# Kernel optimization log

Measured on AMD Instinct MI355X. Metric: run time of the kernel, lower is better.

## Reference

```python
import jax, jax.numpy as jnp
import numpy as np

RESERVOIR_SIZE = 2048
EMBED = 768
N_FRAMES = 256
NUM_CLASSES = 1000
BATCH = 128
SPARSITY = 0.05
SPECTRAL_RADIUS = 0.8


def _init_reservoir(key):
    k1, k2 = jax.random.split(key)
    w = jax.random.normal(k1, (RESERVOIR_SIZE, RESERVOIR_SIZE), dtype=jnp.float32)
    mask = (jax.random.uniform(k2, (RESERVOIR_SIZE, RESERVOIR_SIZE)) < SPARSITY).astype(jnp.float32)
    r = w * mask
    # rescale so spectral radius == SPECTRAL_RADIUS (matches torch eigvals-based init)
    eig = np.linalg.eigvals(np.asarray(r))
    max_abs = np.abs(eig).max()
    return r * (SPECTRAL_RADIUS / jnp.float32(max_abs))


def setup_inputs() -> dict:
    key = jax.random.key(0)
    kx, kr, kin, kout = jax.random.split(key, 4)
    x = jax.random.normal(kx, (BATCH, N_FRAMES, EMBED), dtype=jnp.float32)
    reservoir = _init_reservoir(kr)
    W_in = jax.random.normal(kin, (RESERVOIR_SIZE, EMBED), dtype=jnp.float32) * 0.1
    W_out = jax.random.normal(kout, (NUM_CLASSES, RESERVOIR_SIZE), dtype=jnp.float32) * 0.02
    b_out = jnp.zeros((NUM_CLASSES,), dtype=jnp.float32)
    return {"x": x, "reservoir": reservoir, "W_in": W_in, "W_out": W_out, "b_out": b_out}


def reference(x, reservoir, W_in, W_out, b_out):
    # x: [B, T, E]. Precompute input projections for all frames in one GEMM:
    # u[t] = x[:, t] @ W_in.T  -> [T, B, R]
    u = jnp.einsum("bte,re->tbr", x, W_in)
    state0 = jnp.zeros((x.shape[0], reservoir.shape[0]), dtype=x.dtype)

    def step(state, u_t):
        new_state = jnp.tanh(state @ reservoir.T + u_t)
        return new_state, None

    state, _ = jax.lax.scan(step, state0, u)
    # linear head (dropout is identity in eval mode)
    logits = state @ W_out.T + b_out
    return logits
```

## Files before the change

### kernel.cpp

```cpp
#include <hip/hip_runtime.h>
#include <stdint.h>
#include <stddef.h>

#define BATCH 128
#define NFRAMES 256
#define EMBED 768
#define RES 2048
#define NCLS 1000
#define NWG 256

typedef __attribute__((ext_vector_type(8))) short bf16x8;
typedef __attribute__((ext_vector_type(4))) float f32x4;
typedef unsigned short u16;

__device__ inline u16 f2bf(float f) {
    union { float f; unsigned u; } v; v.f = f;
    unsigned r = v.u + 0x7FFFu + ((v.u >> 16) & 1u);
    return (u16)(r >> 16);
}
__device__ inline float bf2f(u16 h) {
    union { unsigned u; float f; } v; v.u = ((unsigned)h) << 16;
    return v.f;
}
__device__ inline float tanh_fast(float x) {
    float z = __builtin_amdgcn_exp2f(x * 2.885390081777927f);
    return 1.f - 2.f * __builtin_amdgcn_rcpf(z + 1.f);
}

__global__ __launch_bounds__(256) void cvt_kernel(const float* __restrict__ in,
                                                  u16* __restrict__ out, int n4) {
    int i = blockIdx.x * blockDim.x + threadIdx.x;
    int stride = gridDim.x * blockDim.x;
    for (; i < n4; i += stride) {
        float4 v = ((const float4*)in)[i];
        ushort4 o;
        o.x = f2bf(v.x); o.y = f2bf(v.y); o.z = f2bf(v.z); o.w = f2bf(v.w);
        ((ushort4*)out)[i] = o;
    }
}

__global__ __launch_bounds__(512, 1) void recur_kernel(const u16* __restrict__ res,
                                                       const u16* __restrict__ win,
                                                       const u16* __restrict__ xb,
                                                       u16* __restrict__ ring,
                                                       const u16* __restrict__ s0,
                                                       unsigned* __restrict__ flags) {
    __shared__ float part[8][16][66];
    const int lane = threadIdx.x & 63;
    const int w = threadIdx.x >> 6;
    const int rowgrp = (int)(blockIdx.x & 7);
    const int colblk = (int)(blockIdx.x >> 3);
    const int m0 = rowgrp * 16;
    const int n0 = colblk * 64;
    const int lr = lane & 15;
    const int lk = (lane >> 4) * 8;
    const int rb = (lane >> 4) * 4;
    const int kbase = w * 256;
    const int xkbase = w * 96;
    unsigned* myflag = flags + rowgrp * 32 + colblk;
    const unsigned* pollflag = flags + rowgrp * 32 + (lane & 31);

    bf16x8 bfr[4][8];
#pragma unroll
    for (int jf = 0; jf < 4; jf++)
#pragma unroll
        for (int kk = 0; kk < 8; kk++)
            bfr[jf][kk] = *(const bf16x8*)(res + (size_t)(n0 + jf * 16 + lr) * RES + kbase + kk * 32 + lk);

    bf16x8 wfr[4][3];
#pragma unroll
    for (int jf = 0; jf < 4; jf++)
#pragma unroll
        for (int j = 0; j < 3; j++)
            wfr[jf][j] = *(const bf16x8*)(win + (size_t)(n0 + jf * 16 + lr) * EMBED + xkbase + j * 32 + lk);

    const int er = threadIdx.x >> 5;
    const int ec = (threadIdx.x & 31) * 2;
    const size_t gidx = (size_t)(m0 + er) * RES + n0 + ec;
    const u16* xrow = xb + (size_t)(m0 + lr) * NFRAMES * EMBED + xkbase + lk;

    for (int t = 0; t < NFRAMES; t++) {
        const u16* sin = (t == 0) ? s0 : ring + (size_t)(t - 1) * BATCH * RES;
        u16* sout = ring + (size_t)t * BATCH * RES;
        const u16* abase = sin + (size_t)(m0 + lr) * RES + kbase + lk;
        const u16* xp = xrow + (size_t)t * EMBED;

        bf16x8 xa[3];
#pragma unroll
        for (int j = 0; j < 3; j++)
            asm volatile("global_load_dwordx4 %0, %1, off"
                         : "=v"(xa[j]) : "v"(xp + j * 32));
        bf16x8 a[8];
#pragma unroll
        for (int kk = 0; kk < 8; kk++)
            asm volatile("global_load_dwordx4 %0, %1, off"
                         : "=v"(a[kk]) : "v"(abase + kk * 32));

        f32x4 acc[4];
#pragma unroll
        for (int jf = 0; jf < 4; jf++) acc[jf] = (f32x4)0.f;

        asm volatile("s_waitcnt vmcnt(8)" ::: "memory");
        __builtin_amdgcn_sched_barrier(0);
#pragma unroll
        for (int j = 0; j < 3; j++)
#pragma unroll
            for (int jf = 0; jf < 4; jf++)
                acc[jf] = __builtin_amdgcn_mfma_f32_16x16x32_bf16(xa[j], wfr[jf][j], acc[jf], 0, 0, 0);

        asm volatile("s_waitcnt vmcnt(4)" ::: "memory");
        __builtin_amdgcn_sched_barrier(0);
#pragma unroll
        for (int kk = 0; kk < 4; kk++)
#pragma unroll
            for (int jf = 0; jf < 4; jf++)
                acc[jf] = __builtin_amdgcn_mfma_f32_16x16x32_bf16(a[kk], bfr[jf][kk], acc[jf], 0, 0, 0);
        asm volatile("s_waitcnt vmcnt(0)" ::: "memory");
        __builtin_amdgcn_sched_barrier(0);
#pragma unroll
        for (int kk = 4; kk < 8; kk++)
#pragma unroll
            for (int jf = 0; jf < 4; jf++)
                acc[jf] = __builtin_amdgcn_mfma_f32_16x16x32_bf16(a[kk], bfr[jf][kk], acc[jf], 0, 0, 0);

#pragma unroll
        for (int jf = 0; jf < 4; jf++)
#pragma unroll
            for (int q = 0; q < 4; q++)
                part[w][rb + q][jf * 16 + lr] = acc[jf][q];
        __syncthreads();

        float sx = 0.f, sy = 0.f;
#pragma unroll
        for (int ww = 0; ww < 8; ww++) {
            float2 v = *(const float2*)&part[ww][er][ec];
            sx += v.x; sy += v.y;
        }
        float v0 = tanh_fast(sx);
        float v1 = tanh_fast(sy);
        unsigned pk = (unsigned)f2bf(v0) | ((unsigned)f2bf(v1) << 16);
        asm volatile("global_store_dword %0, %1, off sc0 sc1"
                     :: "v"(sout + gidx), "v"(pk) : "memory");

        asm volatile("s_waitcnt vmcnt(0)" ::: "memory");
        __syncthreads();
        if (t != NFRAMES - 1) {
            unsigned stamp = (unsigned)(t + 1);
            if (w == 0) {
                if (lane == 0)
                    asm volatile("global_store_dword %0, %1, off sc0 sc1"
                                 :: "v"(myflag), "v"(stamp) : "memory");
                unsigned f;
                do {
                    asm volatile("global_load_dword %0, %1, off sc0 sc1\n\ts_waitcnt vmcnt(0)"
                                 : "=v"(f) : "v"(pollflag) : "memory");
                    if (__all((int)(f >= stamp))) break;
                    __builtin_amdgcn_s_sleep(2);
                } while (1);
            }
            __syncthreads();
        }
    }
}

__global__ __launch_bounds__(512) void head_kernel(const u16* __restrict__ sin,
                                                   const u16* __restrict__ wout,
                                                   const float* __restrict__ bias,
                                                   float* __restrict__ out) {
    __shared__ float part[8][32][33];
    int lane = threadIdx.x & 63;
    int w = threadIdx.x >> 6;
    int m0 = blockIdx.x * 32;
    int n0 = blockIdx.y * 32;
    int k0 = w * 256;
    int lr = lane & 15;
    int lk = (lane >> 4) * 8;

    f32x4 acc[2][2];
#pragma unroll
    for (int i = 0; i < 2; i++)
#pragma unroll
        for (int j = 0; j < 2; j++) acc[i][j] = (f32x4)0.f;

    for (int kk = k0; kk < k0 + 256; kk += 32) {
        bf16x8 a[2], b[2];
#pragma unroll
        for (int i = 0; i < 2; i++)
            a[i] = *(const bf16x8*)(sin + (size_t)(m0 + i * 16 + lr) * RES + kk + lk);
#pragma unroll
        for (int j = 0; j < 2; j++) {
            int row = n0 + j * 16 + lr;
            if (row > NCLS - 1) row = NCLS - 1;
            b[j] = *(const bf16x8*)(wout + (size_t)row * RES + kk + lk);
        }
#pragma unroll
        for (int i = 0; i < 2; i++)
#pragma unroll
            for (int j = 0; j < 2; j++)
                acc[i][j] = __builtin_amdgcn_mfma_f32_16x16x32_bf16(a[i], b[j], acc[i][j], 0, 0, 0);
    }

    int rowbase = (lane >> 4) * 4;
#pragma unroll
    for (int i = 0; i < 2; i++)
#pragma unroll
        for (int j = 0; j < 2; j++)
#pragma unroll
            for (int q = 0; q < 4; q++)
                part[w][i * 16 + rowbase + q][j * 16 + lr] = acc[i][j][q];

    __syncthreads();

    for (int idx = threadIdx.x; idx < 1024; idx += 512) {
        int r = idx >> 5, c = idx & 31;
        float s = 0.f;
#pragma unroll
        for (int ww = 0; ww < 8; ww++) s += part[ww][r][c];
        int cg = n0 + c;
        if (cg < NCLS)
            out[(size_t)(m0 + r) * NCLS + cg] = s + bias[cg];
    }
}

extern "C" void kernel_launch(void* const* d_in, const int* in_sizes, int n_in,
                              void* d_out, int out_size, void* d_ws, size_t ws_size,
                              hipStream_t stream) {
    const float* x_f    = (const float*)d_in[0];
    const float* res_f  = (const float*)d_in[1];
    const float* win_f  = (const float*)d_in[2];
    const float* wout_f = (const float*)d_in[3];
    const float* bias   = (const float*)d_in[4];
    float* out = (float*)d_out;

    char* ws = (char*)d_ws;
    size_t off = 0;
    auto alloc = [&](size_t bytes) -> void* {
        void* p = ws + off;
        off += (bytes + 255) & ~(size_t)255;
        return p;
    };
    u16* res_b  = (u16*)alloc((size_t)RES * RES * 2);
    u16* win_b  = (u16*)alloc((size_t)RES * EMBED * 2);
    u16* wout_b = (u16*)alloc((size_t)NCLS * RES * 2);
    u16* x_b    = (u16*)alloc((size_t)BATCH * NFRAMES * EMBED * 2);
    u16* ring   = (u16*)alloc((size_t)NFRAMES * BATCH * RES * 2);
    u16* s0     = (u16*)alloc((size_t)BATCH * RES * 2);
    unsigned* flags = (unsigned*)alloc(1024);

    cvt_kernel<<<dim3(1024), dim3(256), 0, stream>>>(res_f, res_b, RES * RES / 4);
    cvt_kernel<<<dim3(512), dim3(256), 0, stream>>>(win_f, win_b, RES * EMBED / 4);
    cvt_kernel<<<dim3(512), dim3(256), 0, stream>>>(wout_f, wout_b, NCLS * RES / 4);
    cvt_kernel<<<dim3(2048), dim3(256), 0, stream>>>(x_f, x_b, BATCH * NFRAMES * EMBED / 4);

    hipMemsetAsync(s0, 0, (size_t)BATCH * RES * 2, stream);
    hipMemsetAsync(flags, 0, 1024, stream);

    void* args[] = { (void*)&res_b, (void*)&win_b, (void*)&x_b, (void*)&ring,
                     (void*)&s0, (void*)&flags };
    hipLaunchCooperativeKernel((const void*)recur_kernel, dim3(NWG), dim3(512),
                               args, 0, stream);

    const u16* sfin = ring + (size_t)(NFRAMES - 1) * BATCH * RES;
    head_kernel<<<dim3(4, 32), dim3(512), 0, stream>>>(sfin, wout_b, bias, out);
}
```

Before: 1.220 ms.

## Replace flag barrier with data-sentinel polling on ring buffer

Drops the per-step flag store and poll barrier between workgroups. Instead the whole ring buffer is filled with 0xFF and consumers spin until the state values they load contain no all-ones words, so the data itself serves as the readiness signal. This removes a flag round-trip and a block barrier from each timestep. In exchange it adds a 128MB memset, reloads whole tiles while polling, and relies on tanh outputs never packing to 0xFFFFFFFF plus on the order in which the bf16 pairs become visible.

```diff
diff --git a/kernel.cpp b/kernel.cpp
--- a/kernel.cpp
+++ b/kernel.cpp
@@ -17,10 +17,6 @@
     union { float f; unsigned u; } v; v.f = f;
     unsigned r = v.u + 0x7FFFu + ((v.u >> 16) & 1u);
     return (u16)(r >> 16);
-}
-__device__ inline float bf2f(u16 h) {
-    union { unsigned u; float f; } v; v.u = ((unsigned)h) << 16;
-    return v.f;
 }
 __device__ inline float tanh_fast(float x) {
     float z = __builtin_amdgcn_exp2f(x * 2.885390081777927f);
@@ -43,8 +39,7 @@
                                                        const u16* __restrict__ win,
                                                        const u16* __restrict__ xb,
                                                        u16* __restrict__ ring,
-                                                       const u16* __restrict__ s0,
-                                                       unsigned* __restrict__ flags) {
+                                                       const u16* __restrict__ s0) {
     __shared__ float part[8][16][66];
     const int lane = threadIdx.x & 63;
     const int w = threadIdx.x >> 6;
@@ -57,8 +52,6 @@
     const int rb = (lane >> 4) * 4;
     const int kbase = w * 256;
     const int xkbase = w * 96;
-    unsigned* myflag = flags + rowgrp * 32 + colblk;
-    const unsigned* pollflag = flags + rowgrp * 32 + (lane & 31);
 
     bf16x8 bfr[4][8];
 #pragma unroll
@@ -85,16 +78,16 @@
         const u16* abase = sin + (size_t)(m0 + lr) * RES + kbase + lk;
         const u16* xp = xrow + (size_t)t * EMBED;
 
+        bf16x8 a[8];
+#pragma unroll
+        for (int kk = 0; kk < 8; kk++)
+            asm volatile("global_load_dwordx4 %0, %1, off sc0 sc1"
+                         : "=v"(a[kk]) : "v"(abase + kk * 32));
         bf16x8 xa[3];
 #pragma unroll
         for (int j = 0; j < 3; j++)
             asm volatile("global_load_dwordx4 %0, %1, off"
                          : "=v"(xa[j]) : "v"(xp + j * 32));
-        bf16x8 a[8];
-#pragma unroll
-        for (int kk = 0; kk < 8; kk++)
-            asm volatile("global_load_dwordx4 %0, %1, off"
-                         : "=v"(a[kk]) : "v"(abase + kk * 32));
 
         f32x4 acc[4];
 #pragma unroll
@@ -102,23 +95,35 @@
 
         asm volatile("s_waitcnt vmcnt(8)" ::: "memory");
         __builtin_amdgcn_sched_barrier(0);
+        asm volatile("s_waitcnt vmcnt(0)" ::: "memory");
+        __builtin_amdgcn_sched_barrier(0);
 #pragma unroll
         for (int j = 0; j < 3; j++)
 #pragma unroll
             for (int jf = 0; jf < 4; jf++)
                 acc[jf] = __builtin_amdgcn_mfma_f32_16x16x32_bf16(xa[j], wfr[jf][j], acc[jf], 0, 0, 0);
 
-        asm volatile("s_waitcnt vmcnt(4)" ::: "memory");
+        while (1) {
+            int ok = 1;
+#pragma unroll
+            for (int kk = 0; kk < 8; kk++) {
+                const unsigned* dw = (const unsigned*)&a[kk];
+#pragma unroll
+                for (int d = 0; d < 4; d++) ok &= (dw[d] != 0xFFFFFFFFu);
+            }
+            if (__all(ok)) break;
+            __builtin_amdgcn_s_sleep(1);
+#pragma unroll
+            for (int kk = 0; kk < 8; kk++)
+                asm volatile("global_load_dwordx4 %0, %1, off sc0 sc1"
+                             : "=v"(a[kk]) : "v"(abase + kk * 32));
+            asm volatile("s_waitcnt vmcnt(0)" ::: "memory");
+            __builtin_amdgcn_sched_barrier(0);
+        }
         __builtin_amdgcn_sched_barrier(0);
-#pragma unroll
-        for (int kk = 0; kk < 4; kk++)
-#pragma unroll
-            for (int jf = 0; jf < 4; jf++)
-                acc[jf] = __builtin_amdgcn_mfma_f32_16x16x32_bf16(a[kk], bfr[jf][kk], acc[jf], 0, 0, 0);
-        asm volatile("s_waitcnt vmcnt(0)" ::: "memory");
-        __builtin_amdgcn_sched_barrier(0);
-#pragma unroll
-        for (int kk = 4; kk < 8; kk++)
+
+#pragma unroll
+        for (int kk = 0; kk < 8; kk++)
 #pragma unroll
             for (int jf = 0; jf < 4; jf++)
                 acc[jf] = __builtin_amdgcn_mfma_f32_16x16x32_bf16(a[kk], bfr[jf][kk], acc[jf], 0, 0, 0);
@@ -141,25 +146,7 @@
         unsigned pk = (unsigned)f2bf(v0) | ((unsigned)f2bf(v1) << 16);
         asm volatile("global_store_dword %0, %1, off sc0 sc1"
                      :: "v"(sout + gidx), "v"(pk) : "memory");
-
-        asm volatile("s_waitcnt vmcnt(0)" ::: "memory");
         __syncthreads();
-        if (t != NFRAMES - 1) {
-            unsigned stamp = (unsigned)(t + 1);
-            if (w == 0) {
-                if (lane == 0)
-                    asm volatile("global_store_dword %0, %1, off sc0 sc1"
-                                 :: "v"(myflag), "v"(stamp) : "memory");
-                unsigned f;
-                do {
-                    asm volatile("global_load_dword %0, %1, off sc0 sc1\n\ts_waitcnt vmcnt(0)"
-                                 : "=v"(f) : "v"(pollflag) : "memory");
-                    if (__all((int)(f >= stamp))) break;
-                    __builtin_amdgcn_s_sleep(2);
-                } while (1);
-            }
-            __syncthreads();
-        }
     }
 }
 
@@ -245,18 +232,16 @@
     u16* x_b    = (u16*)alloc((size_t)BATCH * NFRAMES * EMBED * 2);
     u16* ring   = (u16*)alloc((size_t)NFRAMES * BATCH * RES * 2);
     u16* s0     = (u16*)alloc((size_t)BATCH * RES * 2);
-    unsigned* flags = (unsigned*)alloc(1024);
 
     cvt_kernel<<<dim3(1024), dim3(256), 0, stream>>>(res_f, res_b, RES * RES / 4);
     cvt_kernel<<<dim3(512), dim3(256), 0, stream>>>(win_f, win_b, RES * EMBED / 4);
     cvt_kernel<<<dim3(512), dim3(256), 0, stream>>>(wout_f, wout_b, NCLS * RES / 4);
     cvt_kernel<<<dim3(2048), dim3(256), 0, stream>>>(x_f, x_b, BATCH * NFRAMES * EMBED / 4);
 
+    hipMemsetAsync(ring, 0xFF, (size_t)NFRAMES * BATCH * RES * 2, stream);
     hipMemsetAsync(s0, 0, (size_t)BATCH * RES * 2, stream);
-    hipMemsetAsync(flags, 0, 1024, stream);
-
-    void* args[] = { (void*)&res_b, (void*)&win_b, (void*)&x_b, (void*)&ring,
-                     (void*)&s0, (void*)&flags };
+
+    void* args[] = { (void*)&res_b, (void*)&win_b, (void*)&x_b, (void*)&ring, (void*)&s0 };
     hipLaunchCooperativeKernel((const void*)recur_kernel, dim3(NWG), dim3(512),
                                args, 0, stream);
 
```

Result: slower. 1.734 ms (+42.2%).

## Overlap next-step input projection with grid barrier and signal via LDS counter

Applied to the files above, without the earlier changes.

The per-step input-projection MFMAs and their x loads move out of the critical path: they run for frame t+1 right after the flag is published, so they overlap with the cross-workgroup wait. The flag is now written by whichever wave arrives last at an LDS atomic counter, replacing the block-wide barrier before signalling. The partial-sum buffer is double-buffered so the dropped barrier does not create a read/write hazard. In exchange the kernel uses more LDS, holds extra accumulator registers, and relies on per-wave memory ordering being correct for the publish.

```diff
diff --git a/kernel.cpp b/kernel.cpp
--- a/kernel.cpp
+++ b/kernel.cpp
@@ -17,10 +17,6 @@
     union { float f; unsigned u; } v; v.f = f;
     unsigned r = v.u + 0x7FFFu + ((v.u >> 16) & 1u);
     return (u16)(r >> 16);
-}
-__device__ inline float bf2f(u16 h) {
-    union { unsigned u; float f; } v; v.u = ((unsigned)h) << 16;
-    return v.f;
 }
 __device__ inline float tanh_fast(float x) {
     float z = __builtin_amdgcn_exp2f(x * 2.885390081777927f);
@@ -45,7 +41,8 @@
                                                        u16* __restrict__ ring,
                                                        const u16* __restrict__ s0,
                                                        unsigned* __restrict__ flags) {
-    __shared__ float part[8][16][66];
+    __shared__ float part[2][8][16][66];
+    __shared__ unsigned cnt;
     const int lane = threadIdx.x & 63;
     const int w = threadIdx.x >> 6;
     const int rowgrp = (int)(blockIdx.x & 7);
@@ -60,6 +57,8 @@
     unsigned* myflag = flags + rowgrp * 32 + colblk;
     const unsigned* pollflag = flags + rowgrp * 32 + (lane & 31);
 
+    if (threadIdx.x == 0) cnt = 0;
+
     bf16x8 bfr[4][8];
 #pragma unroll
     for (int jf = 0; jf < 4; jf++)
@@ -79,17 +78,43 @@
     const size_t gidx = (size_t)(m0 + er) * RES + n0 + ec;
     const u16* xrow = xb + (size_t)(m0 + lr) * NFRAMES * EMBED + xkbase + lk;
 
+    f32x4 xacc[4];
+#pragma unroll
+    for (int jf = 0; jf < 4; jf++) xacc[jf] = (f32x4)0.f;
+    {
+        bf16x8 xa[3];
+#pragma unroll
+        for (int j = 0; j < 3; j++)
+            asm volatile("global_load_dwordx4 %0, %1, off"
+                         : "=v"(xa[j]) : "v"(xrow + j * 32));
+        asm volatile("s_waitcnt vmcnt(0)" ::: "memory");
+        __builtin_amdgcn_sched_barrier(0);
+#pragma unroll
+        for (int j = 0; j < 3; j++)
+#pragma unroll
+            for (int jf = 0; jf < 4; jf++)
+                xacc[jf] = __builtin_amdgcn_mfma_f32_16x16x32_bf16(xa[j], wfr[jf][j], xacc[jf], 0, 0, 0);
+    }
+
     for (int t = 0; t < NFRAMES; t++) {
         const u16* sin = (t == 0) ? s0 : ring + (size_t)(t - 1) * BATCH * RES;
         u16* sout = ring + (size_t)t * BATCH * RES;
         const u16* abase = sin + (size_t)(m0 + lr) * RES + kbase + lk;
-        const u16* xp = xrow + (size_t)t * EMBED;
-
-        bf16x8 xa[3];
-#pragma unroll
-        for (int j = 0; j < 3; j++)
-            asm volatile("global_load_dwordx4 %0, %1, off"
-                         : "=v"(xa[j]) : "v"(xp + j * 32));
+        const int cur = t & 1;
+
+        if (t > 0) {
+            if (w == 0) {
+                unsigned f;
+                do {
+                    asm volatile("global_load_dword %0, %1, off sc0 sc1\n\ts_waitcnt vmcnt(0)"
+                                 : "=v"(f) : "v"(pollflag) : "memory");
+                    if (__all((int)(f >= (unsigned)t))) break;
+                    __builtin_amdgcn_s_sleep(1);
+                } while (1);
+            }
+            __syncthreads();
+        }
+
         bf16x8 a[8];
 #pragma unroll
         for (int kk = 0; kk < 8; kk++)
@@ -98,15 +123,7 @@
 
         f32x4 acc[4];
 #pragma unroll
-        for (int jf = 0; jf < 4; jf++) acc[jf] = (f32x4)0.f;
-
-        asm volatile("s_waitcnt vmcnt(8)" ::: "memory");
-        __builtin_amdgcn_sched_barrier(0);
-#pragma unroll
-        for (int j = 0; j < 3; j++)
-#pragma unroll
-            for (int jf = 0; jf < 4; jf++)
-                acc[jf] = __builtin_amdgcn_mfma_f32_16x16x32_bf16(xa[j], wfr[jf][j], acc[jf], 0, 0, 0);
+        for (int jf = 0; jf < 4; jf++) acc[jf] = xacc[jf];
 
         asm volatile("s_waitcnt vmcnt(4)" ::: "memory");
         __builtin_amdgcn_sched_barrier(0);
@@ -127,13 +144,13 @@
         for (int jf = 0; jf < 4; jf++)
 #pragma unroll
             for (int q = 0; q < 4; q++)
-                part[w][rb + q][jf * 16 + lr] = acc[jf][q];
+                part[cur][w][rb + q][jf * 16 + lr] = acc[jf][q];
         __syncthreads();
 
         float sx = 0.f, sy = 0.f;
 #pragma unroll
         for (int ww = 0; ww < 8; ww++) {
-            float2 v = *(const float2*)&part[ww][er][ec];
+            float2 v = *(const float2*)&part[cur][ww][er][ec];
             sx += v.x; sy += v.y;
         }
         float v0 = tanh_fast(sx);
@@ -143,22 +160,30 @@
                      :: "v"(sout + gidx), "v"(pk) : "memory");
 
         asm volatile("s_waitcnt vmcnt(0)" ::: "memory");
-        __syncthreads();
         if (t != NFRAMES - 1) {
-            unsigned stamp = (unsigned)(t + 1);
-            if (w == 0) {
-                if (lane == 0)
+            if (lane == 0) {
+                unsigned old = atomicAdd(&cnt, 1u);
+                if (old == (unsigned)(8 * t + 7)) {
+                    unsigned stamp = (unsigned)(t + 1);
                     asm volatile("global_store_dword %0, %1, off sc0 sc1"
                                  :: "v"(myflag), "v"(stamp) : "memory");
-                unsigned f;
-                do {
-                    asm volatile("global_load_dword %0, %1, off sc0 sc1\n\ts_waitcnt vmcnt(0)"
-                                 : "=v"(f) : "v"(pollflag) : "memory");
-                    if (__all((int)(f >= stamp))) break;
-                    __builtin_amdgcn_s_sleep(2);
-                } while (1);
+                }
             }
-            __syncthreads();
+            const u16* xp = xrow + (size_t)(t + 1) * EMBED;
+            bf16x8 xa[3];
+#pragma unroll
+            for (int j = 0; j < 3; j++)
+                asm volatile("global_load_dwordx4 %0, %1, off"
+                             : "=v"(xa[j]) : "v"(xp + j * 32));
+#pragma unroll
+            for (int jf = 0; jf < 4; jf++) xacc[jf] = (f32x4)0.f;
+            asm volatile("s_waitcnt vmcnt(0)" ::: "memory");
+            __builtin_amdgcn_sched_barrier(0);
+#pragma unroll
+            for (int j = 0; j < 3; j++)
+#pragma unroll
+                for (int jf = 0; jf < 4; jf++)
+                    xacc[jf] = __builtin_amdgcn_mfma_f32_16x16x32_bf16(xa[j], wfr[jf][j], xacc[jf], 0, 0, 0);
         }
     }
 }
```

Measured after the change: 1.132 ms (median of 2 runs). -7.2%, faster.
